# Kernel optimization log

Measured on AMD Instinct MI355X. Metric: run time of the kernel, lower is better.

The kernel has to match this reference:

```python
import jax, jax.numpy as jnp
import numpy as np

IMAGE_W = 1024
IMAGE_H = 1024
MIN_SCORE_THRESHOLD = 0.05
NMS_THRESHOLD = 0.5
MAX_DETECTION_NUM = 100


def setup_inputs() -> dict:
    key = jax.random.key(0)
    k1, k2, k3, k4 = jax.random.split(key, 4)
    B, N, C = 2, 8192, 80
    cls_heads = jax.random.uniform(k1, (B, N, C), jnp.float32)          # post-sigmoid class probs
    reg_heads = jax.random.normal(k2, (B, N, 4), jnp.float32)           # tx,ty,tw,th
    ctr = jax.random.uniform(k3, (B, N, 2), jnp.float32, 0.0, 1024.0)   # anchor centers
    wh = jax.random.uniform(k4, (B, N, 2), jnp.float32, 16.0, 256.0)    # anchor sizes
    anchors = jnp.concatenate([ctr - 0.5 * wh, ctr + 0.5 * wh], axis=-1)  # x1,y1,x2,y2
    return {"cls_heads": cls_heads, "reg_heads": reg_heads, "anchors": anchors}


def _snap_boxes(reg, anchors):
    # reg, anchors: [N, 4]
    awh = anchors[:, 2:] - anchors[:, :2]
    actr = anchors[:, :2] + 0.5 * awh
    factor = jnp.array([0.1, 0.1, 0.2, 0.2], dtype=reg.dtype)
    reg = reg * factor
    pwh = jnp.exp(reg[:, 2:]) * awh
    pctr = reg[:, :2] * awh + actr
    boxes = jnp.concatenate([pctr - 0.5 * pwh, pctr + 0.5 * pwh], axis=1)
    boxes = jax.lax.stop_gradient(boxes).astype(jnp.int32)  # torch .int() truncation
    boxes = boxes.at[:, 0].set(jnp.maximum(boxes[:, 0], 0))
    boxes = boxes.at[:, 1].set(jnp.maximum(boxes[:, 1], 0))
    boxes = boxes.at[:, 2].set(jnp.minimum(boxes[:, 2], IMAGE_W - 1))
    boxes = boxes.at[:, 3].set(jnp.minimum(boxes[:, 3], IMAGE_H - 1))
    return boxes


def _decode_one(cls_head, reg_head, anchor):
    # cls_head: [N, C], reg_head: [N, 4], anchor: [N, 4]
    scores = jnp.max(cls_head, axis=-1)
    classes = jnp.argmax(cls_head, axis=-1).astype(jnp.int32)
    boxes = _snap_boxes(reg_head, anchor)  # int32 [N,4]
    valid = scores > MIN_SCORE_THRESHOLD

    order = jnp.argsort(-scores)  # descending score order
    s = scores[order]
    c = classes[order]
    b = boxes[order]
    v = valid[order]

    bf = b.astype(jnp.float32)
    x1, y1, x2, y2 = bf[:, 0], bf[:, 1], bf[:, 2], bf[:, 3]
    area = jnp.maximum(x2 - x1, 0.0) * jnp.maximum(y2 - y1, 0.0)
    ix1 = jnp.maximum(x1[:, None], x1[None, :])
    iy1 = jnp.maximum(y1[:, None], y1[None, :])
    ix2 = jnp.minimum(x2[:, None], x2[None, :])
    iy2 = jnp.minimum(y2[:, None], y2[None, :])
    inter = jnp.maximum(ix2 - ix1, 0.0) * jnp.maximum(iy2 - iy1, 0.0)
    union = area[:, None] + area[None, :] - inter
    iou = jnp.where(union > 0.0, inter / union, 0.0)  # [N,N]

    N = s.shape[0]
    idx = jnp.arange(N)
    # class-wise suppression: box j (lower score) suppressed by kept box i if IoU>thr
    sup = (iou > NMS_THRESHOLD) & (c[:, None] == c[None, :]) & (idx[None, :] > idx[:, None])

    def body(i, keep):
        return jnp.where(keep[i], keep & ~sup[i], keep)

    keep = jax.lax.fori_loop(0, N, body, v)

    final_scores = jnp.where(keep, s, -1.0)
    top_s, top_i = jax.lax.top_k(final_scores, MAX_DETECTION_NUM)
    ok = top_s > -0.5
    out_scores = jnp.where(ok, top_s, -1.0)
    out_classes = jnp.where(ok, c[top_i], -1)
    out_boxes = jnp.where(ok[:, None], b[top_i], -1)
    return out_scores, out_classes, out_boxes


def reference(cls_heads, reg_heads, anchors):
    # cls_heads: [B,N,C], reg_heads: [B,N,4], anchors: [B,N,4]
    return jax.vmap(_decode_one)(cls_heads, reg_heads, anchors)
```

## Files before the change

kernel.cpp:

```cpp
#include <hip/hip_runtime.h>
#include <stdint.h>

#define NANCH   8192
#define NCLS    80
#define IMW     1024
#define IMH     1024
#define MAXDET  100
#define SCORE_TH 0.05f
#define TAU      0.999691f
#define CAP      512
#define KSENT    0x7FFFFFF0
#define ROWS_PB  64

__device__ __forceinline__ float key_score(uint64_t key) {
    uint32_t m = (uint32_t)(key >> 32);
    uint32_t bits = (m & 0x80000000u) ? (m & 0x7FFFFFFFu) : ~m;
    return __uint_as_float(bits);
}

__global__ __launch_bounds__(256)
void decode_kernel(const float* __restrict__ cls_heads,
                   const float* __restrict__ reg_heads,
                   const float* __restrict__ anchors,
                   int* __restrict__ cnt,
                   uint64_t* __restrict__ wk,
                   uint64_t* __restrict__ wm,
                   ulonglong2* __restrict__ surv) {
    const int tid  = threadIdx.x;
    const int lane = tid & 63;
    const int part = tid & 3;
    const int b    = blockIdx.y;
    const int n    = blockIdx.x * ROWS_PB + (tid >> 2);
    const int row  = b * NANCH + n;

    float best = -1e30f; int bestj = 0;
    {
        const float* rp = cls_heads + (size_t)row * NCLS;
#pragma unroll
        for (int k = 0; k < 5; ++k) {
            int j0 = part * 4 + k * 16;
            float4 v = *reinterpret_cast<const float4*>(rp + j0);
            if (v.x > best) { best = v.x; bestj = j0 + 0; }
            if (v.y > best) { best = v.y; bestj = j0 + 1; }
            if (v.z > best) { best = v.z; bestj = j0 + 2; }
            if (v.w > best) { best = v.w; bestj = j0 + 3; }
        }
    }

    uint32_t ub = __float_as_uint(best);
    uint32_t mono = (ub & 0x80000000u) ? ~ub : (ub | 0x80000000u);
    uint64_t kk = ((uint64_t)mono << 8) | (uint64_t)(255 - bestj);
    {
        uint64_t o = __shfl_xor(kk, 1); if (o > kk) kk = o;
        o = __shfl_xor(kk, 2); if (o > kk) kk = o;
    }

    bool owner = (part == 0);
    uint32_t mono32 = (uint32_t)(kk >> 8);
    int bj = 255 - (int)(kk & 0xFF);

    uint64_t key = 0, meta = 0;
    bool svv = false;
    if (owner) {
        float4 r = reinterpret_cast<const float4*>(reg_heads)[row];
        float4 a = reinterpret_cast<const float4*>(anchors)[row];

        float awx = __fsub_rn(a.z, a.x);
        float awy = __fsub_rn(a.w, a.y);
        float acx = __fadd_rn(a.x, __fmul_rn(0.5f, awx));
        float acy = __fadd_rn(a.y, __fmul_rn(0.5f, awy));
        float rx = __fmul_rn(r.x, 0.1f);
        float ry = __fmul_rn(r.y, 0.1f);
        float rw = __fmul_rn(r.z, 0.2f);
        float rh = __fmul_rn(r.w, 0.2f);
        float pwx = __fmul_rn(expf(rw), awx);
        float pwy = __fmul_rn(expf(rh), awy);
        float pcx = __fadd_rn(__fmul_rn(rx, awx), acx);
        float pcy = __fadd_rn(__fmul_rn(ry, awy), acy);

        int x1 = (int)__fsub_rn(pcx, __fmul_rn(0.5f, pwx));
        int y1 = (int)__fsub_rn(pcy, __fmul_rn(0.5f, pwy));
        int x2 = (int)__fadd_rn(pcx, __fmul_rn(0.5f, pwx));
        int y2 = (int)__fadd_rn(pcy, __fmul_rn(0.5f, pwy));
        x1 = max(x1, 0);
        y1 = max(y1, 0);
        x2 = min(x2, IMW - 1);
        y2 = min(y2, IMH - 1);

        key = ((uint64_t)mono32 << 32)
            | ((uint64_t)((~(uint32_t)n) & 0xFFFFu) << 16)
            | (uint64_t)(uint32_t)bj;
        meta = (uint64_t)(uint16_t)x1
             | ((uint64_t)(uint16_t)y1 << 16)
             | ((uint64_t)(uint16_t)x2 << 32)
             | ((uint64_t)(uint16_t)y2 << 48);

        wk[row] = key;
        wm[row] = meta;

        uint32_t mono_tau = __float_as_uint(TAU) | 0x80000000u;
        svv = (mono32 > mono_tau);
    }

    uint64_t mask = __ballot(svv);
    int rank = __popcll(mask & ((1ULL << lane) - 1ULL));
    int base = 0;
    if (lane == 0 && mask) base = atomicAdd(cnt + b, __popcll(mask));
    base = __shfl(base, 0);
    if (svv) {
        int p = base + rank;
        if (p < CAP) surv[(size_t)b * CAP + p] = make_ulonglong2(key, meta);
    }
}

struct Kept {
    float x1[2], y1[2], x2[2], y2[2], ar[2];
    int   cl[2];
};

__device__ __forceinline__ void nms_try_keep(uint64_t key, uint64_t meta, float s,
                                             int lane, int& nk, Kept& K,
                                             float* __restrict__ out, int b) {
    int cls = (int)(key & 0xFFFFu);
    float cx1 = (float)(short)(meta & 0xFFFFu);
    float cy1 = (float)(short)((meta >> 16) & 0xFFFFu);
    float cx2 = (float)(short)((meta >> 32) & 0xFFFFu);
    float cy2 = (float)(short)((meta >> 48) & 0xFFFFu);
    float ca = fmaxf(cx2 - cx1, 0.f) * fmaxf(cy2 - cy1, 0.f);

    bool supp = false;
#pragma unroll
    for (int r = 0; r < 2; ++r) {
        int slot = lane + 64 * r;
        if (slot < nk && K.cl[r] == cls) {
            float ix1 = fmaxf(K.x1[r], cx1), iy1 = fmaxf(K.y1[r], cy1);
            float ix2 = fminf(K.x2[r], cx2), iy2 = fminf(K.y2[r], cy2);
            float inter = fmaxf(ix2 - ix1, 0.f) * fmaxf(iy2 - iy1, 0.f);
            if (3.f * inter > K.ar[r] + ca) supp = true;
        }
    }
    if (__ballot(supp) != 0ULL) return;

    int rr = nk >> 6, l = nk & 63;
    if (lane == l) {
        if (rr == 0) { K.x1[0]=cx1; K.y1[0]=cy1; K.x2[0]=cx2; K.y2[0]=cy2; K.ar[0]=ca; K.cl[0]=cls; }
        else         { K.x1[1]=cx1; K.y1[1]=cy1; K.x2[1]=cx2; K.y2[1]=cy2; K.ar[1]=ca; K.cl[1]=cls; }
    }
    if (lane == 0) {
        out[b * MAXDET + nk] = s;
        out[2 * MAXDET + b * MAXDET + nk] = (float)cls;
        float* ob = out + 4 * MAXDET + (size_t)(b * MAXDET + nk) * 4;
        ob[0] = cx1; ob[1] = cy1; ob[2] = cx2; ob[3] = cy2;
    }
    ++nk;
}

__global__ __launch_bounds__(256)
void sort_nms_kernel(const int* __restrict__ cnt,
                     const uint64_t* __restrict__ wk,
                     const uint64_t* __restrict__ wm,
                     const ulonglong2* __restrict__ surv,
                     float* __restrict__ out) {
    __shared__ __align__(16) ulonglong2 sv_[CAP];
    __shared__ __align__(16) ulonglong2 sq[CAP];
    __shared__ __align__(16) uint64_t skey[CAP + 16];
    __shared__ float4 kept_box[128];
    __shared__ float  kept_area[128];
    __shared__ int    kept_cls[128];
    __shared__ uint64_t smask[4];
    __shared__ uint64_t sby[4 * 64];
    __shared__ int snk, sdone, sneedfb;
    __shared__ uint64_t fbmap[NANCH / 64];

    const int b = blockIdx.x;
    const int tid = threadIdx.x;
    const int lane = tid & 63;
    const int w = tid >> 6;

    ulonglong2 v0 = surv[(size_t)b * CAP + tid];
    ulonglong2 v1 = surv[(size_t)b * CAP + 256 + tid];
    int c = cnt[b];

    bool overflow = (c > CAP) || (c < 0);
    if (overflow) c = 0;
    const int cpad   = (c + 63) & ~63;
    const int cpad16 = (c + 15) & ~15;

    sv_[tid]       = v0;  skey[tid]       = (tid < c)       ? v0.x : 0ULL;
    sv_[256 + tid] = v1;  skey[256 + tid] = (256 + tid < c) ? v1.x : 0ULL;
    if (tid < 128) kept_cls[tid] = KSENT;
    if (tid == 0) { snk = 0; sdone = 0; sneedfb = overflow ? 1 : 0; }
    __syncthreads();

    for (int i = tid; i < c; i += 256) {
        uint64_t ky = skey[i];
        int r = 0;
        for (int j0 = 0; j0 < cpad16; j0 += 16) {
            int acc = 0;
#pragma unroll
            for (int u = 0; u < 8; ++u) {
                ulonglong2 pr = *reinterpret_cast<const ulonglong2*>(&skey[j0 + 2 * u]);
                acc += (int)(pr.x > ky) + (int)(pr.y > ky);
            }
            r += acc;
        }
        sq[r] = sv_[i];
    }
    for (int i = c + tid; i < cpad; i += 256) sq[i] = make_ulonglong2(0ULL, 0ULL);

    for (int p0 = 0; p0 < cpad; p0 += 64) {
        __syncthreads();
        if (sdone) break;
        const int nk = snk;

        ulonglong2 kv = sq[p0 + lane];
        uint64_t key = kv.x, meta = kv.y;
        float s = key_score(key);
        bool sval = (s > SCORE_TH);
        int cls_c = sval ? (int)(key & 0xFFFFu) : -1;
        float cx1 = (float)(short)(meta & 0xFFFFu);
        float cy1 = (float)(short)((meta >> 16) & 0xFFFFu);
        float cx2 = (float)(short)((meta >> 32) & 0xFFFFu);
        float cy2 = (float)(short)((meta >> 48) & 0xFFFFu);
        float ca = fmaxf(cx2 - cx1, 0.f) * fmaxf(cy2 - cy1, 0.f);

        bool supk = false;
        int kp = (((nk + 3) >> 2) + 7) & ~7;
        for (int k0 = 0; k0 < kp; k0 += 8) {
#pragma unroll
            for (int u = 0; u < 8; ++u) {
                int j = w + 4 * (k0 + u);
                float4 kb = kept_box[j];
                float ka = kept_area[j];
                int kc = kept_cls[j];
                float ix1 = fmaxf(kb.x, cx1), iy1 = fmaxf(kb.y, cy1);
                float ix2 = fminf(kb.z, cx2), iy2 = fminf(kb.w, cy2);
                float inter = fmaxf(ix2 - ix1, 0.f) * fmaxf(iy2 - iy1, 0.f);
                supk |= (kc == cls_c) & (3.f * inter > ka + ca);
            }
        }

        uint64_t sbyw = 0;
#pragma unroll
        for (int u = 0; u < 16; ++u) {
            int t = (w << 4) + u;
            ulonglong2 tv = sq[p0 + t];
            uint64_t tkey = tv.x, tmeta = tv.y;
            float ts = key_score(tkey);
            int tcls = (int)(tkey & 0xFFFFu);
            float tx1 = (float)(short)(tmeta & 0xFFFFu);
            float ty1 = (float)(short)((tmeta >> 16) & 0xFFFFu);
            float tx2 = (float)(short)((tmeta >> 32) & 0xFFFFu);
            float ty2 = (float)(short)((tmeta >> 48) & 0xFFFFu);
            float ta = fmaxf(tx2 - tx1, 0.f) * fmaxf(ty2 - ty1, 0.f);
            float ix1 = fmaxf(tx1, cx1), iy1 = fmaxf(ty1, cy1);
            float ix2 = fminf(tx2, cx2), iy2 = fminf(ty2, cy2);
            float inter = fmaxf(ix2 - ix1, 0.f) * fmaxf(iy2 - iy1, 0.f);
            bool sup = (t < lane) && (ts > SCORE_TH) && (tcls == cls_c)
                       && (3.f * inter > ta + ca);
            sbyw |= ((uint64_t)sup) << t;
        }

        uint64_t mk = __ballot(supk);
        if (lane == 0) smask[w] = mk;
        sby[(w << 6) + lane] = sbyw;
        __syncthreads();

        if (w == 0) {
            uint64_t supkAll = smask[0] | smask[1] | smask[2] | smask[3];
            uint64_t supBy = sby[lane] | sby[64 + lane] | sby[128 + lane] | sby[192 + lane];
            bool alive0 = sval && !((supkAll >> lane) & 1ULL);

            uint64_t aliveCand = __ballot(alive0);
            uint64_t aliveMask;
            if (__ballot(supBy != 0ULL) == 0ULL) {
                aliveMask = aliveCand;
            } else {
                uint64_t killed = 0;
                for (int t = 0; t < 64; ++t) {
                    uint64_t kill_t = __ballot((supBy >> t) & 1ULL);
                    bool talive = ((aliveCand >> t) & 1ULL) && !((killed >> t) & 1ULL);
                    if (talive) killed |= kill_t;
                }
                aliveMask = aliveCand & ~killed;
            }

            int myrank = __popcll(aliveMask & ((1ULL << lane) - 1ULL));
            bool keepme = ((aliveMask >> lane) & 1ULL) && (nk + myrank < MAXDET);
            if (keepme) {
                int slot = nk + myrank;
                kept_box[slot]  = make_float4(cx1, cy1, cx2, cy2);
                kept_area[slot] = ca;
                kept_cls[slot]  = cls_c;
                out[b * MAXDET + slot] = s;
                out[2 * MAXDET + b * MAXDET + slot] = (float)cls_c;
                float* ob = out + 4 * MAXDET + (size_t)(b * MAXDET + slot) * 4;
                ob[0] = cx1; ob[1] = cy1; ob[2] = cx2; ob[3] = cy2;
            }
            int navail = __popcll(aliveMask);
            int room = MAXDET - nk;
            int nk2 = nk + ((navail < room) ? navail : room);
            uint64_t invalid = __ballot(!sval);
            if (lane == 0) {
                snk = nk2;
                if (nk2 >= MAXDET) sdone = 1;
                else if (invalid) { sneedfb = 1; sdone = 1; }
            }
        }
    }
    __syncthreads();

    int nk = snk;
    bool need_fb = sneedfb || (!sdone && nk < MAXDET);

    if (tid >= 64) return;

    if (need_fb) {
        const uint64_t* wkb = wk + (size_t)b * NANCH;
        const uint64_t* wmb = wm + (size_t)b * NANCH;
        for (int i = lane; i < NANCH / 64; i += 64) fbmap[i] = 0ULL;
        __builtin_amdgcn_wave_barrier();

        nk = 0;
        Kept K;
        K.cl[0] = K.cl[1] = -1;
        K.x1[0]=K.y1[0]=K.x2[0]=K.y2[0]=K.ar[0]=0.f;
        K.x1[1]=K.y1[1]=K.x2[1]=K.y2[1]=K.ar[1]=0.f;

        for (int iter = 0; iter < NANCH; ++iter) {
            uint64_t mybest = 0; int myq = -1;
            for (int q = lane; q < NANCH; q += 64) {
                bool cons = (fbmap[q >> 6] >> (q & 63)) & 1ULL;
                uint64_t kk2 = wkb[q];
                if (!cons && kk2 > mybest) { mybest = kk2; myq = q; }
            }
            uint64_t best = mybest;
#pragma unroll
            for (int j = 32; j; j >>= 1) {
                uint64_t o = __shfl_xor(best, j);
                if (o > best) best = o;
            }
            if (best == 0ULL) break;
            float s = key_score(best);
            if (!(s > SCORE_TH)) break;
            uint64_t msk = __ballot(mybest == best);
            int wl = __ffsll((unsigned long long)msk) - 1;
            int q = __shfl(myq, wl);
            if (lane == wl) fbmap[q >> 6] |= (1ULL << (q & 63));
            uint64_t cm = wmb[q];
            nms_try_keep(best, cm, s, lane, nk, K, out, b);
            if (nk == MAXDET) break;
            __builtin_amdgcn_wave_barrier();
        }
    }

    for (int t = nk + lane; t < MAXDET; t += 64) {
        out[b * MAXDET + t] = -1.f;
        out[2 * MAXDET + b * MAXDET + t] = -1.f;
        float* ob = out + 4 * MAXDET + (size_t)(b * MAXDET + t) * 4;
        ob[0] = -1.f; ob[1] = -1.f; ob[2] = -1.f; ob[3] = -1.f;
    }
}

extern "C" void kernel_launch(void* const* d_in, const int* in_sizes, int n_in,
                              void* d_out, int out_size, void* d_ws, size_t ws_size,
                              hipStream_t stream) {
    (void)in_sizes; (void)n_in; (void)out_size; (void)ws_size;
    const float* cls_heads = (const float*)d_in[0];
    const float* reg_heads = (const float*)d_in[1];
    const float* anchors   = (const float*)d_in[2];
    float* out = (float*)d_out;

    char* w = (char*)d_ws;
    int*        cnt  = (int*)w;
    uint64_t*   wk   = (uint64_t*)(w + 1024);
    uint64_t*   wm   = (uint64_t*)(w + 1024 + 131072);
    ulonglong2* surv = (ulonglong2*)(w + 1024 + 262144);

    hipMemsetAsync(cnt, 0, 2 * sizeof(int), stream);
    decode_kernel<<<dim3(NANCH / ROWS_PB, 2), 256, 0, stream>>>(cls_heads, reg_heads, anchors,
                                                                cnt, wk, wm, surv);
    sort_nms_kernel<<<dim3(2), 256, 0, stream>>>(cnt, wk, wm, surv, out);
}
```

Baseline: 24.21 us.

## Fuse decode and sort/NMS into one kernel via last-block ticket

Merges the decode kernel and the sort/NMS kernel into a single launch. Each block writes its survivors to its own slot plus a count, then takes an atomic ticket, and the last block of each batch runs the prefix scan, gather, sort and NMS. This removes the memset and the second kernel launch, and it replaces the global survivor atomic with block-local compaction. The ticket counter is never reset and relies on modulo NBLK wrapping. The fused kernel also carries the NMS shared memory in every block, which may reduce occupancy during decode.

```diff
diff --git a/kernel.cpp b/kernel.cpp
--- a/kernel.cpp
+++ b/kernel.cpp
@@ -3,6 +3,7 @@
 
 #define NANCH   8192
 #define NCLS    80
+#define NBLK    128
 #define IMW     1024
 #define IMH     1024
 #define MAXDET  100
@@ -10,7 +11,6 @@
 #define TAU      0.999691f
 #define CAP      512
 #define KSENT    0x7FFFFFF0
-#define ROWS_PB  64
 
 __device__ __forceinline__ float key_score(uint64_t key) {
     uint32_t m = (uint32_t)(key >> 32);
@@ -18,20 +18,83 @@
     return __uint_as_float(bits);
 }
 
+struct Kept {
+    float x1[2], y1[2], x2[2], y2[2], ar[2];
+    int   cl[2];
+};
+
+__device__ __forceinline__ void nms_try_keep(uint64_t key, uint64_t meta, float s,
+                                             int lane, int& nk, Kept& K,
+                                             float* __restrict__ out, int b) {
+    int cls = (int)(key & 0xFFFFu);
+    float cx1 = (float)(short)(meta & 0xFFFFu);
+    float cy1 = (float)(short)((meta >> 16) & 0xFFFFu);
+    float cx2 = (float)(short)((meta >> 32) & 0xFFFFu);
+    float cy2 = (float)(short)((meta >> 48) & 0xFFFFu);
+    float ca = fmaxf(cx2 - cx1, 0.f) * fmaxf(cy2 - cy1, 0.f);
+
+    bool supp = false;
+#pragma unroll
+    for (int r = 0; r < 2; ++r) {
+        int slot = lane + 64 * r;
+        if (slot < nk && K.cl[r] == cls) {
+            float ix1 = fmaxf(K.x1[r], cx1), iy1 = fmaxf(K.y1[r], cy1);
+            float ix2 = fminf(K.x2[r], cx2), iy2 = fminf(K.y2[r], cy2);
+            float inter = fmaxf(ix2 - ix1, 0.f) * fmaxf(iy2 - iy1, 0.f);
+            if (3.f * inter > K.ar[r] + ca) supp = true;
+        }
+    }
+    if (__ballot(supp) != 0ULL) return;
+
+    int rr = nk >> 6, l = nk & 63;
+    if (lane == l) {
+        if (rr == 0) { K.x1[0]=cx1; K.y1[0]=cy1; K.x2[0]=cx2; K.y2[0]=cy2; K.ar[0]=ca; K.cl[0]=cls; }
+        else         { K.x1[1]=cx1; K.y1[1]=cy1; K.x2[1]=cx2; K.y2[1]=cy2; K.ar[1]=ca; K.cl[1]=cls; }
+    }
+    if (lane == 0) {
+        out[b * MAXDET + nk] = s;
+        out[2 * MAXDET + b * MAXDET + nk] = (float)cls;
+        float* ob = out + 4 * MAXDET + (size_t)(b * MAXDET + nk) * 4;
+        ob[0] = cx1; ob[1] = cy1; ob[2] = cx2; ob[3] = cy2;
+    }
+    ++nk;
+}
+
 __global__ __launch_bounds__(256)
-void decode_kernel(const float* __restrict__ cls_heads,
-                   const float* __restrict__ reg_heads,
-                   const float* __restrict__ anchors,
-                   int* __restrict__ cnt,
-                   uint64_t* __restrict__ wk,
-                   uint64_t* __restrict__ wm,
-                   ulonglong2* __restrict__ surv) {
+void fused_kernel(const float* __restrict__ cls_heads,
+                  const float* __restrict__ reg_heads,
+                  const float* __restrict__ anchors,
+                  unsigned* __restrict__ ticket,
+                  int* __restrict__ blkcnt,
+                  uint64_t* __restrict__ wk,
+                  uint64_t* __restrict__ wm,
+                  ulonglong2* __restrict__ surv,
+                  float* __restrict__ out) {
+    __shared__ ulonglong2 lsurv[64];
+    __shared__ int lcnt, lastflag;
+    __shared__ __align__(16) ulonglong2 sv_[CAP];
+    __shared__ __align__(16) ulonglong2 sq[CAP];
+    __shared__ __align__(16) uint64_t skey[CAP + 16];
+    __shared__ float4 kept_box[128];
+    __shared__ float  kept_area[128];
+    __shared__ int    kept_cls[128];
+    __shared__ uint64_t smask[4];
+    __shared__ uint64_t sby[4 * 64];
+    __shared__ int soff[NBLK], scnt[NBLK], stotal;
+    __shared__ int snk, sdone, sneedfb;
+    __shared__ uint64_t fbmap[NANCH / 64];
+
     const int tid  = threadIdx.x;
     const int lane = tid & 63;
+    const int w    = tid >> 6;
     const int part = tid & 3;
+    const int blk  = blockIdx.x;
     const int b    = blockIdx.y;
-    const int n    = blockIdx.x * ROWS_PB + (tid >> 2);
+    const int n    = blk * 64 + (tid >> 2);
     const int row  = b * NANCH + n;
+
+    if (tid == 0) lcnt = 0;
+    __syncthreads();
 
     float best = -1e30f; int bestj = 0;
     {
@@ -46,7 +109,6 @@
             if (v.w > best) { best = v.w; bestj = j0 + 3; }
         }
     }
-
     uint32_t ub = __float_as_uint(best);
     uint32_t mono = (ub & 0x80000000u) ? ~ub : (ub | 0x80000000u);
     uint64_t kk = ((uint64_t)mono << 8) | (uint64_t)(255 - bestj);
@@ -55,13 +117,10 @@
         o = __shfl_xor(kk, 2); if (o > kk) kk = o;
     }
 
-    bool owner = (part == 0);
-    uint32_t mono32 = (uint32_t)(kk >> 8);
-    int bj = 255 - (int)(kk & 0xFF);
-
-    uint64_t key = 0, meta = 0;
-    bool svv = false;
-    if (owner) {
+    if (part == 0) {
+        uint32_t mono32 = (uint32_t)(kk >> 8);
+        int bj = 255 - (int)(kk & 0xFF);
+
         float4 r = reinterpret_cast<const float4*>(reg_heads)[row];
         float4 a = reinterpret_cast<const float4*>(anchors)[row];
 
@@ -87,109 +146,75 @@
         x2 = min(x2, IMW - 1);
         y2 = min(y2, IMH - 1);
 
-        key = ((uint64_t)mono32 << 32)
-            | ((uint64_t)((~(uint32_t)n) & 0xFFFFu) << 16)
-            | (uint64_t)(uint32_t)bj;
-        meta = (uint64_t)(uint16_t)x1
-             | ((uint64_t)(uint16_t)y1 << 16)
-             | ((uint64_t)(uint16_t)x2 << 32)
-             | ((uint64_t)(uint16_t)y2 << 48);
+        uint64_t key = ((uint64_t)mono32 << 32)
+                     | ((uint64_t)((~(uint32_t)n) & 0xFFFFu) << 16)
+                     | (uint64_t)(uint32_t)bj;
+        uint64_t meta = (uint64_t)(uint16_t)x1
+                      | ((uint64_t)(uint16_t)y1 << 16)
+                      | ((uint64_t)(uint16_t)x2 << 32)
+                      | ((uint64_t)(uint16_t)y2 << 48);
 
         wk[row] = key;
         wm[row] = meta;
 
         uint32_t mono_tau = __float_as_uint(TAU) | 0x80000000u;
-        svv = (mono32 > mono_tau);
-    }
-
-    uint64_t mask = __ballot(svv);
-    int rank = __popcll(mask & ((1ULL << lane) - 1ULL));
-    int base = 0;
-    if (lane == 0 && mask) base = atomicAdd(cnt + b, __popcll(mask));
-    base = __shfl(base, 0);
-    if (svv) {
-        int p = base + rank;
-        if (p < CAP) surv[(size_t)b * CAP + p] = make_ulonglong2(key, meta);
-    }
-}
-
-struct Kept {
-    float x1[2], y1[2], x2[2], y2[2], ar[2];
-    int   cl[2];
-};
-
-__device__ __forceinline__ void nms_try_keep(uint64_t key, uint64_t meta, float s,
-                                             int lane, int& nk, Kept& K,
-                                             float* __restrict__ out, int b) {
-    int cls = (int)(key & 0xFFFFu);
-    float cx1 = (float)(short)(meta & 0xFFFFu);
-    float cy1 = (float)(short)((meta >> 16) & 0xFFFFu);
-    float cx2 = (float)(short)((meta >> 32) & 0xFFFFu);
-    float cy2 = (float)(short)((meta >> 48) & 0xFFFFu);
-    float ca = fmaxf(cx2 - cx1, 0.f) * fmaxf(cy2 - cy1, 0.f);
-
-    bool supp = false;
-#pragma unroll
-    for (int r = 0; r < 2; ++r) {
-        int slot = lane + 64 * r;
-        if (slot < nk && K.cl[r] == cls) {
-            float ix1 = fmaxf(K.x1[r], cx1), iy1 = fmaxf(K.y1[r], cy1);
-            float ix2 = fminf(K.x2[r], cx2), iy2 = fminf(K.y2[r], cy2);
-            float inter = fmaxf(ix2 - ix1, 0.f) * fmaxf(iy2 - iy1, 0.f);
-            if (3.f * inter > K.ar[r] + ca) supp = true;
-        }
-    }
-    if (__ballot(supp) != 0ULL) return;
-
-    int rr = nk >> 6, l = nk & 63;
-    if (lane == l) {
-        if (rr == 0) { K.x1[0]=cx1; K.y1[0]=cy1; K.x2[0]=cx2; K.y2[0]=cy2; K.ar[0]=ca; K.cl[0]=cls; }
-        else         { K.x1[1]=cx1; K.y1[1]=cy1; K.x2[1]=cx2; K.y2[1]=cy2; K.ar[1]=ca; K.cl[1]=cls; }
-    }
-    if (lane == 0) {
-        out[b * MAXDET + nk] = s;
-        out[2 * MAXDET + b * MAXDET + nk] = (float)cls;
-        float* ob = out + 4 * MAXDET + (size_t)(b * MAXDET + nk) * 4;
-        ob[0] = cx1; ob[1] = cy1; ob[2] = cx2; ob[3] = cy2;
-    }
-    ++nk;
-}
-
-__global__ __launch_bounds__(256)
-void sort_nms_kernel(const int* __restrict__ cnt,
-                     const uint64_t* __restrict__ wk,
-                     const uint64_t* __restrict__ wm,
-                     const ulonglong2* __restrict__ surv,
-                     float* __restrict__ out) {
-    __shared__ __align__(16) ulonglong2 sv_[CAP];
-    __shared__ __align__(16) ulonglong2 sq[CAP];
-    __shared__ __align__(16) uint64_t skey[CAP + 16];
-    __shared__ float4 kept_box[128];
-    __shared__ float  kept_area[128];
-    __shared__ int    kept_cls[128];
-    __shared__ uint64_t smask[4];
-    __shared__ uint64_t sby[4 * 64];
-    __shared__ int snk, sdone, sneedfb;
-    __shared__ uint64_t fbmap[NANCH / 64];
-
-    const int b = blockIdx.x;
-    const int tid = threadIdx.x;
-    const int lane = tid & 63;
-    const int w = tid >> 6;
-
-    ulonglong2 v0 = surv[(size_t)b * CAP + tid];
-    ulonglong2 v1 = surv[(size_t)b * CAP + 256 + tid];
-    int c = cnt[b];
-
+        if (mono32 > mono_tau) {
+            int p = atomicAdd(&lcnt, 1);
+            lsurv[p] = make_ulonglong2(key, meta);
+        }
+    }
+    __syncthreads();
+
+    const int myc = lcnt;
+    if (tid < myc) surv[((size_t)b * NBLK + blk) * 64 + tid] = lsurv[tid];
+    if (tid == 0) blkcnt[b * NBLK + blk] = myc;
+
+    __threadfence();
+    __syncthreads();
+    if (tid == 0) {
+        unsigned old = __hip_atomic_fetch_add(ticket + b, 1u, __ATOMIC_ACQ_REL,
+                                              __HIP_MEMORY_SCOPE_AGENT);
+        lastflag = ((old & (NBLK - 1)) == (NBLK - 1)) ? 1 : 0;
+    }
+    __syncthreads();
+    if (!lastflag) return;
+
+    if (tid < 64) {
+        int a0 = blkcnt[b * NBLK + 2 * tid];
+        int a1 = blkcnt[b * NBLK + 2 * tid + 1];
+        int s = a0 + a1;
+#pragma unroll
+        for (int j = 1; j < 64; j <<= 1) {
+            int o = __shfl_up(s, j);
+            if (lane >= j) s += o;
+        }
+        int excl = s - (a0 + a1);
+        soff[2 * tid] = excl;
+        soff[2 * tid + 1] = excl + a0;
+        scnt[2 * tid] = a0;
+        scnt[2 * tid + 1] = a1;
+        if (tid == 63) stotal = s;
+    }
+    if (tid < 128) kept_cls[tid] = KSENT;
+    if (tid == 0) { snk = 0; sdone = 0; sneedfb = 0; }
+    __syncthreads();
+
+    int c = stotal;
     bool overflow = (c > CAP) || (c < 0);
-    if (overflow) c = 0;
+    if (overflow) { c = 0; if (tid == 0) sneedfb = 1; }
     const int cpad   = (c + 63) & ~63;
     const int cpad16 = (c + 15) & ~15;
 
-    sv_[tid]       = v0;  skey[tid]       = (tid < c)       ? v0.x : 0ULL;
-    sv_[256 + tid] = v1;  skey[256 + tid] = (256 + tid < c) ? v1.x : 0ULL;
-    if (tid < 128) kept_cls[tid] = KSENT;
-    if (tid == 0) { snk = 0; sdone = 0; sneedfb = overflow ? 1 : 0; }
+    for (int idx = tid; idx < NANCH; idx += 256) {
+        int ch = idx >> 6, k = idx & 63;
+        if (k < scnt[ch] && !overflow) {
+            ulonglong2 v = surv[((size_t)b * NBLK + ch) * 64 + k];
+            int pos = soff[ch] + k;
+            sv_[pos]  = v;
+            skey[pos] = v.x;
+        }
+    }
+    for (int i = c + tid; i < cpad16; i += 256) skey[i] = 0ULL;
     __syncthreads();
 
     for (int i = tid; i < c; i += 256) {
@@ -334,21 +359,21 @@
                 uint64_t kk2 = wkb[q];
                 if (!cons && kk2 > mybest) { mybest = kk2; myq = q; }
             }
-            uint64_t best = mybest;
+            uint64_t best2 = mybest;
 #pragma unroll
             for (int j = 32; j; j >>= 1) {
-                uint64_t o = __shfl_xor(best, j);
-                if (o > best) best = o;
-            }
-            if (best == 0ULL) break;
-            float s = key_score(best);
+                uint64_t o = __shfl_xor(best2, j);
+                if (o > best2) best2 = o;
+            }
+            if (best2 == 0ULL) break;
+            float s = key_score(best2);
             if (!(s > SCORE_TH)) break;
-            uint64_t msk = __ballot(mybest == best);
+            uint64_t msk = __ballot(mybest == best2);
             int wl = __ffsll((unsigned long long)msk) - 1;
             int q = __shfl(myq, wl);
             if (lane == wl) fbmap[q >> 6] |= (1ULL << (q & 63));
             uint64_t cm = wmb[q];
-            nms_try_keep(best, cm, s, lane, nk, K, out, b);
+            nms_try_keep(best2, cm, s, lane, nk, K, out, b);
             if (nk == MAXDET) break;
             __builtin_amdgcn_wave_barrier();
         }
@@ -372,13 +397,12 @@
     float* out = (float*)d_out;
 
     char* w = (char*)d_ws;
-    int*        cnt  = (int*)w;
-    uint64_t*   wk   = (uint64_t*)(w + 1024);
-    uint64_t*   wm   = (uint64_t*)(w + 1024 + 131072);
-    ulonglong2* surv = (ulonglong2*)(w + 1024 + 262144);
-
-    hipMemsetAsync(cnt, 0, 2 * sizeof(int), stream);
-    decode_kernel<<<dim3(NANCH / ROWS_PB, 2), 256, 0, stream>>>(cls_heads, reg_heads, anchors,
-                                                                cnt, wk, wm, surv);
-    sort_nms_kernel<<<dim3(2), 256, 0, stream>>>(cnt, wk, wm, surv, out);
+    unsigned*   ticket = (unsigned*)w;
+    int*        blkcnt = (int*)(w + 1024);
+    uint64_t*   wk     = (uint64_t*)(w + 4096);
+    uint64_t*   wm     = (uint64_t*)(w + 4096 + 131072);
+    ulonglong2* surv   = (ulonglong2*)(w + 4096 + 262144);
+
+    fused_kernel<<<dim3(NBLK, 2), 256, 0, stream>>>(cls_heads, reg_heads, anchors,
+                                                    ticket, blkcnt, wk, wm, surv, out);
 }
```

Measured after the change: 43.38 us. 1.79x slower.
